# Kernel optimization log

Measured on AMD Instinct MI355X. Metric: run time of the kernel, lower is better.

## Reference

```python
import jax, jax.numpy as jnp
import numpy as np

EPS = 1e-08

def setup_inputs() -> dict:
    key = jax.random.key(0)
    k1, k2, k3 = jax.random.split(key, 3)
    b, cin, cout, ksz, h, w = 16, 256, 256, 3, 64, 64
    return {
        "x": jax.random.normal(k1, (b, cin, h, w), dtype=jnp.float32),
        "s": jax.random.normal(k2, (b, cin), dtype=jnp.float32),
        "weight": jax.random.normal(k3, (cout, cin, ksz, ksz), dtype=jnp.float32),
    }

def reference(x, s, weight):
    # x: [b, cin, h, w]; s: [b, cin]; weight: [cout, cin, k, k]
    b, cin, h, w = x.shape
    cout, _, ksz, _ = weight.shape
    pad = ksz // 2
    # demodulate pre-normalization of weight and style
    wn = weight * jax.lax.rsqrt(jnp.mean(jnp.square(weight), axis=(1, 2, 3), keepdims=True))
    sn = s * jax.lax.rsqrt(jnp.mean(jnp.square(s)))
    # per-sample modulation: [b, cout, cin, k, k]
    wmod = wn[None, :, :, :, :] * sn[:, None, :, None, None]
    # demodulation: normalize each output filter per sample
    sigma_inv = jax.lax.rsqrt(jnp.sum(jnp.square(wmod), axis=(2, 3, 4), keepdims=True) + EPS)
    wmod = wmod * sigma_inv
    # batch-grouped conv: input [1, b*cin, h, w], weight [b*cout, cin, k, k]
    xg = x.reshape(1, b * cin, h, w)
    wg = wmod.reshape(b * cout, cin, ksz, ksz)
    y = jax.lax.conv_general_dilated(
        xg, wg,
        window_strides=(1, 1),
        padding=[(pad, pad), (pad, pad)],
        feature_group_count=b,
        dimension_numbers=("NCHW", "OIHW", "NCHW"),
    )
    return y.reshape(b, cout, h, w)
```

## Files before the change

### kernel.cpp

```cpp
#include <hip/hip_runtime.h>
#include <hip/hip_bf16.h>

#define EPS 1e-8f
#define B_  16
#define CIN 256
#define COUT 256
#define HW 64

typedef __bf16 bf16x8 __attribute__((ext_vector_type(8)));
typedef float  f32x4  __attribute__((ext_vector_type(4)));

__device__ __forceinline__ void async16(void* lds, const void* g) {
    __builtin_amdgcn_global_load_lds(
        (const __attribute__((address_space(1))) unsigned int*)g,
        (__attribute__((address_space(3))) unsigned int*)lds,
        16, 0, 0);
}

__global__ __launch_bounds__(256) void stats_kernel(const float* __restrict__ w,
                                                    const float* __restrict__ s,
                                                    float* __restrict__ wsq,
                                                    float* __restrict__ wn_scale,
                                                    float* __restrict__ ssum_out) {
    __shared__ float smem[4];
    const int t = threadIdx.x;
    const int lane = t & 63, wid = t >> 6;
    if (blockIdx.x == 256) {
        float v = 0.f;
        for (int i = t; i < B_ * CIN; i += 256) { float sv = s[i]; v += sv * sv; }
        for (int off = 32; off > 0; off >>= 1) v += __shfl_down(v, off, 64);
        if (lane == 0) smem[wid] = v;
        __syncthreads();
        if (t == 0) ssum_out[0] = smem[0] + smem[1] + smem[2] + smem[3];
        return;
    }
    const int co = blockIdx.x;
    const float* wp = w + ((size_t)co * CIN + t) * 9;
    float q = 0.f;
#pragma unroll
    for (int tp = 0; tp < 9; ++tp) { float wv = wp[tp]; q += wv * wv; }
    wsq[co * CIN + t] = q;
    float v = q;
    for (int off = 32; off > 0; off >>= 1) v += __shfl_down(v, off, 64);
    if (lane == 0) smem[wid] = v;
    __syncthreads();
    if (t == 0) wn_scale[co] = rsqrtf((smem[0] + smem[1] + smem[2] + smem[3]) / 2304.f);
}

__global__ __launch_bounds__(256) void wmod_kernel(const float* __restrict__ w,
                                                   const float* __restrict__ s,
                                                   const float* __restrict__ wsq,
                                                   const float* __restrict__ wn_scale,
                                                   const float* __restrict__ ssum,
                                                   __bf16* __restrict__ wfull) {
    __shared__ float smem[4];
    __shared__ float coef_s;
    const int co = blockIdx.x;
    const int b  = blockIdx.y;
    const int ci = threadIdx.x;
    const int lane = ci & 63, wid = ci >> 6;
    const float sv = s[b * CIN + ci];
    float v = sv * sv * wsq[co * CIN + ci];
    for (int off = 32; off > 0; off >>= 1) v += __shfl_down(v, off, 64);
    if (lane == 0) smem[wid] = v;
    __syncthreads();
    if (ci == 0) {
        float S = smem[0] + smem[1] + smem[2] + smem[3];
        float sn2 = (float)(B_ * CIN) / ssum[0];
        float wn = wn_scale[co];
        coef_s = wn * sqrtf(sn2) * rsqrtf(wn * wn * sn2 * S + EPS);
    }
    __syncthreads();
    const float sc = sv * coef_s;
    const float* wp = w + ((size_t)co * CIN + ci) * 9;
    float wv[9];
#pragma unroll
    for (int tp = 0; tp < 9; ++tp) wv[tp] = wp[tp];
    const size_t obase = ((size_t)b * 9) * 65536 + (size_t)(ci >> 5) * 8192
                       + (size_t)co * 32 + (ci & 31);
#pragma unroll
    for (int tap = 0; tap < 9; ++tap)
        wfull[obase + (size_t)tap * 65536] = (__bf16)(wv[tap] * sc);
}

#define TP 258
__global__ __launch_bounds__(256) void xbf2_kernel(const float* __restrict__ x,
                                                   __bf16* __restrict__ xbf) {
    __shared__ __bf16 xs[64 * TP];
    const int row = blockIdx.x;
    const int b   = blockIdx.y;
    const int t   = threadIdx.x;
    const float* xbase = x + ((size_t)b * CIN * HW + row) * HW;
#pragma unroll
    for (int k = 0; k < 16; ++k) {
        int idx = k * 256 + t;
        int ci = idx >> 4;
        int c4 = (idx & 15) * 4;
        float4 v = *(const float4*)(xbase + (size_t)ci * (HW * HW) + c4);
        xs[(c4 + 0) * TP + ci] = (__bf16)v.x;
        xs[(c4 + 1) * TP + ci] = (__bf16)v.y;
        xs[(c4 + 2) * TP + ci] = (__bf16)v.z;
        xs[(c4 + 3) * TP + ci] = (__bf16)v.w;
    }
    __syncthreads();
    uint* orow = (uint*)(xbf + (((size_t)b * HW + row) * 66) * CIN);
#pragma unroll
    for (int k = 0; k < 17; ++k) {
        int idx = k * 256 + t;
        if (idx < 66 * 64) {
            int col = idx >> 6;
            int ci4 = (idx & 63) * 4;
            uint u0 = 0, u1 = 0;
            if (col != 0 && col != 65) {
                u0 = *(const uint*)&xs[(col - 1) * TP + ci4];
                u1 = *(const uint*)&xs[(col - 1) * TP + ci4 + 2];
            }
            orow[(col * CIN + ci4) >> 1] = u0;
            orow[((col * CIN + ci4) >> 1) + 1] = u1;
        }
    }
}

__global__ __launch_bounds__(256, 3) void conv_mfma3(const __bf16* __restrict__ xbf,
                                                     const __bf16* __restrict__ zrow,
                                                     const __bf16* __restrict__ wfull,
                                                     float* __restrict__ out) {
    __shared__ __attribute__((aligned(16))) __bf16 xs[2][800 * 8];

    const int bid = blockIdx.x;
    const int b    = (bid & 7) + ((bid >= 512) ? 8 : 0);
    const int row0 = (bid >> 3) & 63;
    const int t = threadIdx.x;
    const int wy = t >> 6, lane = t & 63;
    const int m16 = lane & 15, q = lane >> 4;

    const __bf16* gsrc[4];
    unsigned ldsoff[4];
    bool val[4];
#pragma unroll
    for (int i = 0; i < 4; ++i) {
        int slot = i * 256 + t;
        val[i] = slot < 800;
        int qq  = slot / 200;
        int rem = slot - qq * 200;
        int irow = rem / 66;
        int col  = rem - irow * 66;
        const __bf16* g;
        if (!val[i] || rem >= 198) {
            g = zrow;
        } else {
            int gr = row0 - 1 + irow;
            if ((unsigned)gr < 64u)
                g = xbf + (((size_t)b * HW + gr) * 66 + col) * CIN + qq * 8;
            else
                g = zrow + col * CIN + qq * 8;
        }
        gsrc[i] = g;
        ldsoff[i] = (unsigned)slot * 16;
    }

#pragma unroll
    for (int i = 0; i < 4; ++i)
        if (val[i]) async16((char*)xs[0] + ldsoff[i], gsrc[i]);

    f32x4 acc[4][4] = {};
    const __bf16* abase = wfull + (size_t)b * 589824
                        + (size_t)(wy * 64 + m16) * 32 + q * 8;

    for (int cc = 0; cc < 8; ++cc) {
        __syncthreads();
        if (cc < 7) {
#pragma unroll
            for (int i = 0; i < 4; ++i)
                if (val[i]) async16((char*)xs[(cc + 1) & 1] + ldsoff[i], gsrc[i] + cc * 32 + 32);
        }
        const __bf16* wb = abase + (size_t)cc * 8192;
        const __bf16* xcur = xs[cc & 1];

        bf16x8 afc[4];
#pragma unroll
        for (int i = 0; i < 4; ++i)
            afc[i] = *(const bf16x8*)(wb + i * 512);

#pragma unroll
        for (int tap = 0; tap < 9; ++tap) {
            bf16x8 afn[4];
            if (tap < 8) {
#pragma unroll
                for (int i = 0; i < 4; ++i)
                    afn[i] = *(const bf16x8*)(wb + (size_t)(tap + 1) * 65536 + i * 512);
            }
            const int dr = tap / 3, dc = tap % 3;
            bf16x8 bfr[4];
            const int rb = (q * 200 + dr * 66 + (m16 + dc)) * 8;
#pragma unroll
            for (int j = 0; j < 4; ++j)
                bfr[j] = *(const bf16x8*)&xcur[rb + j * 16 * 8];
            __builtin_amdgcn_s_setprio(1);
#pragma unroll
            for (int i = 0; i < 4; ++i)
#pragma unroll
                for (int j = 0; j < 4; ++j)
                    acc[i][j] = __builtin_amdgcn_mfma_f32_16x16x32_bf16(afc[i], bfr[j], acc[i][j], 0, 0, 0);
            __builtin_amdgcn_s_setprio(0);
            if (tap < 8) {
#pragma unroll
                for (int i = 0; i < 4; ++i) afc[i] = afn[i];
            }
        }
    }

#pragma unroll
    for (int i = 0; i < 4; ++i) {
        const int cobase = wy * 64 + i * 16 + q * 4;
#pragma unroll
        for (int reg = 0; reg < 4; ++reg) {
            float* op = out + ((size_t)b * COUT + (cobase + reg)) * (HW * HW) + row0 * HW;
#pragma unroll
            for (int j = 0; j < 4; ++j)
                op[j * 16 + m16] = acc[i][j][reg];
        }
    }
}

extern "C" void kernel_launch(void* const* d_in, const int* in_sizes, int n_in,
                              void* d_out, int out_size, void* d_ws, size_t ws_size,
                              hipStream_t stream) {
    const float* x = (const float*)d_in[0];
    const float* s = (const float*)d_in[1];
    const float* w = (const float*)d_in[2];
    float* out = (float*)d_out;

    float* ws = (float*)d_ws;
    float*  ssum     = ws;
    float*  wn_scale = ws + 16;
    float*  wsq      = ws + 512;
    __bf16* wfull    = (__bf16*)(ws + 70656);
    __bf16* zrow     = (__bf16*)(ws + 4789248);
    __bf16* xbf      = (__bf16*)(ws + 4797696);

    hipMemsetAsync(zrow, 0, 33792, stream);
    stats_kernel<<<257, 256, 0, stream>>>(w, s, wsq, wn_scale, ssum);
    wmod_kernel<<<dim3(COUT, B_), 256, 0, stream>>>(w, s, wsq, wn_scale, ssum, wfull);
    xbf2_kernel<<<dim3(64, B_), 256, 0, stream>>>(x, xbf);
    conv_mfma3<<<1024, 256, 0, stream>>>(xbf, zrow, wfull, out);
}
```

Baseline: 216.5 us.

## Drop padded columns from bf16 input, pack channel pairs, prefetch LDS fragments across taps

The input conversion kernel now packs two channels per 32-bit LDS word with a skewed index and writes unpadded 64-column rows as 16-byte stores. The conv kernel takes left and right zero padding from the zero row buffer instead of stored padding columns. The conv main loop now software-pipelines the B-fragment LDS reads one tap ahead and prefetches the next chunk's first A fragments across the chunk boundary. This aims to cut conversion traffic and hide LDS and global latency behind the MFMAs, at the cost of more registers per thread, which may lower occupancy under the 3-block launch bound.

```diff
diff --git a/kernel.cpp b/kernel.cpp
--- a/kernel.cpp
+++ b/kernel.cpp
@@ -83,41 +83,44 @@
         wfull[obase + (size_t)tap * 65536] = (__bf16)(wv[tap] * sc);
 }
 
-#define TP 258
+__device__ __forceinline__ uint pack2(float lo, float hi) {
+    __bf16 a = (__bf16)lo, b = (__bf16)hi;
+    unsigned short ua = __builtin_bit_cast(unsigned short, a);
+    unsigned short ub = __builtin_bit_cast(unsigned short, b);
+    return ((uint)ub << 16) | (uint)ua;
+}
+
 __global__ __launch_bounds__(256) void xbf2_kernel(const float* __restrict__ x,
                                                    __bf16* __restrict__ xbf) {
-    __shared__ __bf16 xs[64 * TP];
+    __shared__ uint xsd[64 * 160];
     const int row = blockIdx.x;
     const int b   = blockIdx.y;
     const int t   = threadIdx.x;
     const float* xbase = x + ((size_t)b * CIN * HW + row) * HW;
 #pragma unroll
-    for (int k = 0; k < 16; ++k) {
-        int idx = k * 256 + t;
-        int ci = idx >> 4;
-        int c4 = (idx & 15) * 4;
-        float4 v = *(const float4*)(xbase + (size_t)ci * (HW * HW) + c4);
-        xs[(c4 + 0) * TP + ci] = (__bf16)v.x;
-        xs[(c4 + 1) * TP + ci] = (__bf16)v.y;
-        xs[(c4 + 2) * TP + ci] = (__bf16)v.z;
-        xs[(c4 + 3) * TP + ci] = (__bf16)v.w;
-    }
-    __syncthreads();
-    uint* orow = (uint*)(xbf + (((size_t)b * HW + row) * 66) * CIN);
-#pragma unroll
-    for (int k = 0; k < 17; ++k) {
-        int idx = k * 256 + t;
-        if (idx < 66 * 64) {
-            int col = idx >> 6;
-            int ci4 = (idx & 63) * 4;
-            uint u0 = 0, u1 = 0;
-            if (col != 0 && col != 65) {
-                u0 = *(const uint*)&xs[(col - 1) * TP + ci4];
-                u1 = *(const uint*)&xs[(col - 1) * TP + ci4 + 2];
-            }
-            orow[(col * CIN + ci4) >> 1] = u0;
-            orow[((col * CIN + ci4) >> 1) + 1] = u1;
-        }
+    for (int k = 0; k < 8; ++k) {
+        int p   = k * 256 + t;
+        int ci2 = p >> 4;
+        int c4  = (p & 15) * 4;
+        const float* src = xbase + (size_t)(2 * ci2) * (HW * HW) + c4;
+        float4 v0 = *(const float4*)src;
+        float4 v1 = *(const float4*)(src + HW * HW);
+        const int dj = ci2 + (ci2 >> 2);
+#pragma unroll
+        for (int i = 0; i < 4; ++i)
+            xsd[(c4 + i) * 160 + dj] = pack2((&v0.x)[i], (&v1.x)[i]);
+    }
+    __syncthreads();
+    __bf16* orow = xbf + (((size_t)b * HW + row) * 64) * CIN;
+#pragma unroll
+    for (int k = 0; k < 8; ++k) {
+        int o   = k * 256 + t;
+        int col = o >> 5;
+        int u   = o & 31;
+        const uint* rp = &xsd[col * 160 + 5 * u];
+        uint a0 = rp[0], a1 = rp[1], a2 = rp[2], a3 = rp[3];
+        uint4 vv; vv.x = a0; vv.y = a1; vv.z = a2; vv.w = a3;
+        *(uint4*)&orow[(size_t)col * CIN + u * 8] = vv;
     }
 }
 
@@ -145,15 +148,14 @@
         int rem = slot - qq * 200;
         int irow = rem / 66;
         int col  = rem - irow * 66;
+        int gr = row0 - 1 + irow;
         const __bf16* g;
         if (!val[i] || rem >= 198) {
             g = zrow;
+        } else if ((unsigned)gr < 64u && col != 0 && col != 65) {
+            g = xbf + (((size_t)b * HW + gr) * 64 + (col - 1)) * CIN + qq * 8;
         } else {
-            int gr = row0 - 1 + irow;
-            if ((unsigned)gr < 64u)
-                g = xbf + (((size_t)b * HW + gr) * 66 + col) * CIN + qq * 8;
-            else
-                g = zrow + col * CIN + qq * 8;
+            g = zrow + col * CIN + qq * 8;
         }
         gsrc[i] = g;
         ldsoff[i] = (unsigned)slot * 16;
@@ -167,43 +169,56 @@
     const __bf16* abase = wfull + (size_t)b * 589824
                         + (size_t)(wy * 64 + m16) * 32 + q * 8;
 
+    bf16x8 afc[4], bfc[4];
+#pragma unroll
+    for (int i = 0; i < 4; ++i)
+        afc[i] = *(const bf16x8*)(abase + i * 512);
+
     for (int cc = 0; cc < 8; ++cc) {
+        const __bf16* wb = abase + (size_t)cc * 8192;
         __syncthreads();
         if (cc < 7) {
 #pragma unroll
             for (int i = 0; i < 4; ++i)
                 if (val[i]) async16((char*)xs[(cc + 1) & 1] + ldsoff[i], gsrc[i] + cc * 32 + 32);
         }
-        const __bf16* wb = abase + (size_t)cc * 8192;
         const __bf16* xcur = xs[cc & 1];
-
-        bf16x8 afc[4];
-#pragma unroll
-        for (int i = 0; i < 4; ++i)
-            afc[i] = *(const bf16x8*)(wb + i * 512);
-
+        {
+            const int rb = (q * 200 + m16) * 8;
+#pragma unroll
+            for (int j = 0; j < 4; ++j)
+                bfc[j] = *(const bf16x8*)&xcur[rb + j * 128];
+        }
 #pragma unroll
         for (int tap = 0; tap < 9; ++tap) {
-            bf16x8 afn[4];
+            bf16x8 afn[4], bfn[4];
             if (tap < 8) {
 #pragma unroll
                 for (int i = 0; i < 4; ++i)
                     afn[i] = *(const bf16x8*)(wb + (size_t)(tap + 1) * 65536 + i * 512);
+                const int dr = (tap + 1) / 3, dc = (tap + 1) % 3;
+                const int rb = (q * 200 + dr * 66 + m16 + dc) * 8;
+#pragma unroll
+                for (int j = 0; j < 4; ++j)
+                    bfn[j] = *(const bf16x8*)&xcur[rb + j * 128];
+            } else if (cc < 7) {
+#pragma unroll
+                for (int i = 0; i < 4; ++i)
+                    afn[i] = *(const bf16x8*)(wb + 8192 + i * 512);
             }
-            const int dr = tap / 3, dc = tap % 3;
-            bf16x8 bfr[4];
-            const int rb = (q * 200 + dr * 66 + (m16 + dc)) * 8;
-#pragma unroll
-            for (int j = 0; j < 4; ++j)
-                bfr[j] = *(const bf16x8*)&xcur[rb + j * 16 * 8];
             __builtin_amdgcn_s_setprio(1);
 #pragma unroll
             for (int i = 0; i < 4; ++i)
 #pragma unroll
                 for (int j = 0; j < 4; ++j)
-                    acc[i][j] = __builtin_amdgcn_mfma_f32_16x16x32_bf16(afc[i], bfr[j], acc[i][j], 0, 0, 0);
+                    acc[i][j] = __builtin_amdgcn_mfma_f32_16x16x32_bf16(afc[i], bfc[j], acc[i][j], 0, 0, 0);
             __builtin_amdgcn_s_setprio(0);
             if (tap < 8) {
+#pragma unroll
+                for (int i = 0; i < 4; ++i) afc[i] = afn[i];
+#pragma unroll
+                for (int j = 0; j < 4; ++j) bfc[j] = bfn[j];
+            } else if (cc < 7) {
 #pragma unroll
                 for (int i = 0; i < 4; ++i) afc[i] = afn[i];
             }
@@ -237,9 +252,9 @@
     float*  wsq      = ws + 512;
     __bf16* wfull    = (__bf16*)(ws + 70656);
     __bf16* zrow     = (__bf16*)(ws + 4789248);
-    __bf16* xbf      = (__bf16*)(ws + 4797696);
-
-    hipMemsetAsync(zrow, 0, 33792, stream);
+    __bf16* xbf      = (__bf16*)(ws + 4798464);
+
+    hipMemsetAsync(zrow, 0, 36864, stream);
     stats_kernel<<<257, 256, 0, stream>>>(w, s, wsq, wn_scale, ssum);
     wmod_kernel<<<dim3(COUT, B_), 256, 0, stream>>>(w, s, wsq, wn_scale, ssum, wfull);
     xbf2_kernel<<<dim3(64, B_), 256, 0, stream>>>(x, xbf);
```

Result: no change. 217.7 us (+0.6%).
